# Kernel optimization log

Hardware: AMD Instinct MI355X
Metric: run time of the kernel (lower is better)

Reference implementation:

```python
import jax, jax.numpy as jnp
import numpy as np

N_NODES = 100000
N_EDGES = 1600000
NUM_GRAPHS = 64
D = 128      # num_node_features
H = 256      # hidden_dim
OUT = 1      # output_dim
GA = 6       # num_graph_attributes


def setup_inputs() -> dict:
    key = jax.random.key(0)
    ks = jax.random.split(key, 20)
    p = lambda k, shape: (jax.random.normal(k, shape, jnp.float32) * 0.02)
    return {
        "x": jax.random.normal(ks[0], (N_NODES, D), jnp.float32),
        "edge_index": jax.random.randint(ks[1], (2, N_EDGES), 0, N_NODES),
        "batch": jnp.sort(jax.random.randint(ks[2], (N_NODES,), 0, NUM_GRAPHS)),
        "graph_attr": jax.random.normal(ks[3], (NUM_GRAPHS, GA), jnp.float32),
        # conv1 MLP: Linear(D->H), ReLU, Linear(H->H)
        "w1a": p(ks[4], (D, H)), "b1a": p(ks[5], (H,)),
        "w1b": p(ks[6], (H, H)), "b1b": p(ks[7], (H,)),
        # conv2 MLP: Linear(H->H), ReLU, Linear(H->H)
        "w2a": p(ks[8], (H, H)), "b2a": p(ks[9], (H,)),
        "w2b": p(ks[10], (H, H)), "b2b": p(ks[11], (H,)),
        # head
        "wf1": p(ks[12], (H + GA, H)), "bf1": p(ks[13], (H,)),
        "wf2": p(ks[14], (H, OUT)), "bf2": p(ks[15], (OUT,)),
    }


def _gin_conv(x, src, dst, wa, ba, wb, bb):
    # GINConv with default eps=0: MLP((1+0)*x_i + sum_{j->i} x_j)
    agg = jax.ops.segment_sum(x[src], dst, num_segments=N_NODES)  # [N, d]
    h = x + agg
    h = jax.nn.relu(h @ wa + ba)
    return h @ wb + bb


def reference(x, edge_index, batch, graph_attr,
              w1a, b1a, w1b, b1b, w2a, b2a, w2b, b2b,
              wf1, bf1, wf2, bf2):
    src, dst = edge_index[0], edge_index[1]
    h = jax.nn.relu(_gin_conv(x, src, dst, w1a, b1a, w1b, b1b))  # [N, H]
    h = _gin_conv(h, src, dst, w2a, b2a, w2b, b2b)               # [N, H]
    # global mean pool per graph
    sums = jax.ops.segment_sum(h, batch, num_segments=NUM_GRAPHS)          # [G, H]
    cnts = jax.ops.segment_sum(jnp.ones((h.shape[0], 1), h.dtype), batch,
                               num_segments=NUM_GRAPHS)                    # [G, 1]
    pooled = sums / jnp.maximum(cnts, 1.0)
    g = jnp.concatenate([pooled, graph_attr.reshape(-1, GA)], axis=1)      # [G, H+GA]
    g = jax.nn.relu(g @ wf1 + bf1)
    return g @ wf2 + bf2                                                   # [G, OUT]
```

## Files before the change

kernel.cpp:

```cpp
#include <hip/hip_runtime.h>

#define N_NODES 100000
#define N_EDGES 1600000
#define NGRAPH  64
#define DIN     128
#define HID     256
#define GA      6

#define NBUCK  196
#define BSHIFT 9
#define BCAP   10240

typedef __attribute__((ext_vector_type(8))) short bf16x8;
typedef __attribute__((ext_vector_type(4))) float f32x4;

__device__ __forceinline__ unsigned short f2bf(float f) {
  unsigned int u = __float_as_uint(f);
  u += 0x7fffu + ((u >> 16) & 1u);
  return (unsigned short)(u >> 16);
}
__device__ __forceinline__ float bf_lo(unsigned int u) { return __uint_as_float(u << 16); }
__device__ __forceinline__ float bf_hi(unsigned int u) { return __uint_as_float(u & 0xffff0000u); }
__device__ __forceinline__ unsigned int packbf(float lo, float hi) {
  return (unsigned int)f2bf(lo) | ((unsigned int)f2bf(hi) << 16);
}

__device__ __forceinline__ void gload16(const void* g, void* l) {
  __builtin_amdgcn_global_load_lds(
      (const __attribute__((address_space(1))) unsigned int*)g,
      (__attribute__((address_space(3))) unsigned int*)l, 16, 0, 0);
}


__global__ __launch_bounds__(256) void cvt_all(const float* __restrict__ x,
                                               const float* __restrict__ w1a,
                                               const float* __restrict__ w1b,
                                               const float* __restrict__ w2a,
                                               const float* __restrict__ w2b,
                                               unsigned short* __restrict__ xo,
                                               unsigned short* __restrict__ o1a,
                                               unsigned short* __restrict__ o1b,
                                               unsigned short* __restrict__ o2a,
                                               unsigned short* __restrict__ o2b) {
  int bid = blockIdx.x, tid = threadIdx.x;
  if (bid < 12500) {
    size_t idx = ((size_t)bid * 256 + tid) * 4;
    float4 v = *(const float4*)&x[idx];
    ushort4 o;
    o.x = f2bf(v.x); o.y = f2bf(v.y); o.z = f2bf(v.z); o.w = f2bf(v.w);
    *(ushort4*)&xo[idx] = o;
    return;
  }
  bid -= 12500;
  const float* in; unsigned short* out; int shift, idx;
  if (bid < 128)      { in = w1a; out = o1a; shift = 7; idx = bid * 256 + tid; }
  else if (bid < 384) { in = w1b; out = o1b; shift = 8; idx = (bid - 128) * 256 + tid; }
  else if (bid < 640) { in = w2a; out = o2a; shift = 8; idx = (bid - 384) * 256 + tid; }
  else                { in = w2b; out = o2b; shift = 8; idx = (bid - 640) * 256 + tid; }
  int K = 1 << shift;
  int n = idx >> shift;
  int k = idx & (K - 1);
  out[idx] = f2bf(in[(size_t)k * HID + n]);
}


__global__ __launch_bounds__(256) void bin_kernel(const int* __restrict__ esrc,
                                                  const int* __restrict__ edst,
                                                  int* __restrict__ cursor,
                                                  unsigned int* __restrict__ tmp) {
  __shared__ unsigned int pk[4096];
  __shared__ unsigned char bkb[4096];
  __shared__ int hist[NBUCK], lbase[NBUCK + 1], gbase[NBUCK], lcur[NBUCK];
  const int tid = threadIdx.x;
  const int lane = tid & 63;
  const int ebase = blockIdx.x * 4096;
  const int n = min(4096, N_EDGES - ebase);
  if (tid < NBUCK) hist[tid] = 0;
  __syncthreads();
  unsigned int pkv[16]; int bk[16];
#pragma unroll
  for (int i = 0; i < 16; i++) {
    int e = ebase + i * 256 + tid;
    bk[i] = -1;
    if (e < N_EDGES) {
      int s = esrc[e], d = edst[e];
      bk[i] = d >> BSHIFT;
      pkv[i] = (unsigned int)s | ((unsigned int)(d & ((1 << BSHIFT) - 1)) << 17);
      atomicAdd(&hist[bk[i]], 1);
    }
  }
  __syncthreads();
  if (tid < 64) {
    int i0 = 4 * tid;
    int a0 = (i0 + 0 < NBUCK) ? hist[i0 + 0] : 0;
    int a1 = (i0 + 1 < NBUCK) ? hist[i0 + 1] : 0;
    int a2 = (i0 + 2 < NBUCK) ? hist[i0 + 2] : 0;
    int a3 = (i0 + 3 < NBUCK) ? hist[i0 + 3] : 0;
    int p = a0 + a1 + a2 + a3, sc = p;
#pragma unroll
    for (int off = 1; off < 64; off <<= 1) {
      int t = __shfl_up(sc, off);
      if (lane >= off) sc += t;
    }
    int excl = sc - p;
    if (i0 + 0 < NBUCK) lbase[i0 + 0] = excl;
    if (i0 + 1 < NBUCK) lbase[i0 + 1] = excl + a0;
    if (i0 + 2 < NBUCK) lbase[i0 + 2] = excl + a0 + a1;
    if (i0 + 3 < NBUCK) lbase[i0 + 3] = excl + a0 + a1 + a2;
    if (tid == 63) lbase[NBUCK] = sc;
  }
  __syncthreads();
  if (tid < NBUCK) {
    int c = hist[tid];
    gbase[tid] = c ? atomicAdd(&cursor[tid], c) : 0;
    lcur[tid] = lbase[tid];
  }
  __syncthreads();
#pragma unroll
  for (int i = 0; i < 16; i++) {
    if (bk[i] >= 0) {
      int pos = atomicAdd(&lcur[bk[i]], 1);
      pk[pos] = pkv[i];
      bkb[pos] = (unsigned char)bk[i];
    }
  }
  __syncthreads();
#pragma unroll
  for (int i = 0; i < 16; i++) {
    int idx = i * 256 + tid;
    if (idx < n) {
      int b = bkb[idx];
      tmp[(size_t)b * BCAP + gbase[b] + (idx - lbase[b])] = pk[idx];
    }
  }
}


__global__ __launch_bounds__(512) void sort_kernel(const unsigned int* __restrict__ tmp,
                                                   const int* __restrict__ cnt,
                                                   int* __restrict__ csr,
                                                   int* __restrict__ ssrc) {
  __shared__ int nhist[512], ncur[512];
  __shared__ int bb[NBUCK];
  __shared__ int wsum[8];
  const int b = blockIdx.x;
  const int tid = threadIdx.x;
  const int lane = tid & 63, wid = tid >> 6;
  if (tid < 64) {
    int i0 = 4 * tid;
    int a0 = (i0 + 0 < NBUCK) ? cnt[i0 + 0] : 0;
    int a1 = (i0 + 1 < NBUCK) ? cnt[i0 + 1] : 0;
    int a2 = (i0 + 2 < NBUCK) ? cnt[i0 + 2] : 0;
    int a3 = (i0 + 3 < NBUCK) ? cnt[i0 + 3] : 0;
    int p = a0 + a1 + a2 + a3, sc = p;
#pragma unroll
    for (int off = 1; off < 64; off <<= 1) {
      int t = __shfl_up(sc, off);
      if (lane >= off) sc += t;
    }
    int excl = sc - p;
    if (i0 + 0 < NBUCK) bb[i0 + 0] = excl;
    if (i0 + 1 < NBUCK) bb[i0 + 1] = excl + a0;
    if (i0 + 2 < NBUCK) bb[i0 + 2] = excl + a0 + a1;
    if (i0 + 3 < NBUCK) bb[i0 + 3] = excl + a0 + a1 + a2;
  }
  nhist[tid] = 0;
  __syncthreads();
  const int myCnt = cnt[b];
  const int ebase = bb[b];
  const unsigned int* srcp = tmp + (size_t)b * BCAP;
  for (int i = tid; i < myCnt; i += 512)
    atomicAdd(&nhist[srcp[i] >> 17], 1);
  __syncthreads();
  int v = nhist[tid];
  int sc = v;
#pragma unroll
  for (int off = 1; off < 64; off <<= 1) {
    int t = __shfl_up(sc, off);
    if (lane >= off) sc += t;
  }
  if (lane == 63) wsum[wid] = sc;
  __syncthreads();
  if (tid < 8) {
    int ws = wsum[tid];
#pragma unroll
    for (int off = 1; off < 8; off <<= 1) {
      int t = __shfl_up(ws, off);
      if (tid >= off) ws += t;
    }
    wsum[tid] = ws;
  }
  __syncthreads();
  int excl = ((wid > 0) ? wsum[wid - 1] : 0) + sc - v;
  ncur[tid] = excl;
  int node0 = (b << BSHIFT) + tid;
  if (node0 < N_NODES) csr[node0] = ebase + excl;
  if (b == 0 && tid == 0) csr[N_NODES] = N_EDGES;
  __syncthreads();
  for (int i = tid; i < myCnt; i += 512) {
    unsigned int pe = srcp[i];
    int pos = atomicAdd(&ncur[pe >> 17], 1);
    ssrc[ebase + pos] = (int)(pe & 0x1FFFF);
  }
}


__global__ __launch_bounds__(256) void agg1_kernel(const uint2* __restrict__ x,
                                                   const int* __restrict__ csr,
                                                   const int* __restrict__ ssrc,
                                                   uint2* __restrict__ out) {
  int node = blockIdx.x * 4 + (threadIdx.x >> 6);
  int lane = threadIdx.x & 63;
  int half = lane >> 5;
  int dl   = lane & 31;
  float a0 = 0.f, a1 = 0.f, a2 = 0.f, a3 = 0.f;
  if (half == 0) {
    uint2 u = x[(size_t)node * 32 + dl];
    a0 = bf_lo(u.x); a1 = bf_hi(u.x); a2 = bf_lo(u.y); a3 = bf_hi(u.y);
  }
  int s = csr[node], e = csr[node + 1];
  int i = s;
  for (; i + 8 <= e; i += 8) {
    int s0 = ssrc[i + half],     s1 = ssrc[i + 2 + half];
    int s2 = ssrc[i + 4 + half], s3 = ssrc[i + 6 + half];
    uint2 v0 = x[(size_t)s0 * 32 + dl];
    uint2 v1 = x[(size_t)s1 * 32 + dl];
    uint2 v2 = x[(size_t)s2 * 32 + dl];
    uint2 v3 = x[(size_t)s3 * 32 + dl];
    a0 += bf_lo(v0.x) + bf_lo(v1.x) + bf_lo(v2.x) + bf_lo(v3.x);
    a1 += bf_hi(v0.x) + bf_hi(v1.x) + bf_hi(v2.x) + bf_hi(v3.x);
    a2 += bf_lo(v0.y) + bf_lo(v1.y) + bf_lo(v2.y) + bf_lo(v3.y);
    a3 += bf_hi(v0.y) + bf_hi(v1.y) + bf_hi(v2.y) + bf_hi(v3.y);
  }
  for (; i + 2 <= e; i += 2) {
    int sn = ssrc[i + half];
    uint2 v = x[(size_t)sn * 32 + dl];
    a0 += bf_lo(v.x); a1 += bf_hi(v.x);
    a2 += bf_lo(v.y); a3 += bf_hi(v.y);
  }
  if (i < e && half == 0) {
    uint2 v = x[(size_t)ssrc[i] * 32 + dl];
    a0 += bf_lo(v.x); a1 += bf_hi(v.x);
    a2 += bf_lo(v.y); a3 += bf_hi(v.y);
  }
  a0 += __shfl_xor(a0, 32);
  a1 += __shfl_xor(a1, 32);
  a2 += __shfl_xor(a2, 32);
  a3 += __shfl_xor(a3, 32);
  if (half == 0) {
    uint2 o;
    o.x = packbf(a0, a1);
    o.y = packbf(a2, a3);
    out[(size_t)node * 32 + dl] = o;
  }
}

__global__ __launch_bounds__(256) void agg2_kernel(const uint2* __restrict__ x,
                                                   const int* __restrict__ csr,
                                                   const int* __restrict__ ssrc,
                                                   uint2* __restrict__ out) {
  int node = blockIdx.x * 4 + (threadIdx.x >> 6);
  int lane = threadIdx.x & 63;
  uint2 u = x[(size_t)node * 64 + lane];
  float a0 = bf_lo(u.x), a1 = bf_hi(u.x), a2 = bf_lo(u.y), a3 = bf_hi(u.y);
  int s = csr[node], e = csr[node + 1];
  int i = s;
  for (; i + 8 <= e; i += 8) {
    int n0 = ssrc[i],     n1 = ssrc[i + 1], n2 = ssrc[i + 2], n3 = ssrc[i + 3];
    int n4 = ssrc[i + 4], n5 = ssrc[i + 5], n6 = ssrc[i + 6], n7 = ssrc[i + 7];
    uint2 v0 = x[(size_t)n0 * 64 + lane];
    uint2 v1 = x[(size_t)n1 * 64 + lane];
    uint2 v2 = x[(size_t)n2 * 64 + lane];
    uint2 v3 = x[(size_t)n3 * 64 + lane];
    uint2 v4 = x[(size_t)n4 * 64 + lane];
    uint2 v5 = x[(size_t)n5 * 64 + lane];
    uint2 v6 = x[(size_t)n6 * 64 + lane];
    uint2 v7 = x[(size_t)n7 * 64 + lane];
    a0 += (bf_lo(v0.x) + bf_lo(v1.x)) + (bf_lo(v2.x) + bf_lo(v3.x)) +
          (bf_lo(v4.x) + bf_lo(v5.x)) + (bf_lo(v6.x) + bf_lo(v7.x));
    a1 += (bf_hi(v0.x) + bf_hi(v1.x)) + (bf_hi(v2.x) + bf_hi(v3.x)) +
          (bf_hi(v4.x) + bf_hi(v5.x)) + (bf_hi(v6.x) + bf_hi(v7.x));
    a2 += (bf_lo(v0.y) + bf_lo(v1.y)) + (bf_lo(v2.y) + bf_lo(v3.y)) +
          (bf_lo(v4.y) + bf_lo(v5.y)) + (bf_lo(v6.y) + bf_lo(v7.y));
    a3 += (bf_hi(v0.y) + bf_hi(v1.y)) + (bf_hi(v2.y) + bf_hi(v3.y)) +
          (bf_hi(v4.y) + bf_hi(v5.y)) + (bf_hi(v6.y) + bf_hi(v7.y));
  }
  for (; i < e; i++) {
    uint2 v = x[(size_t)ssrc[i] * 64 + lane];
    a0 += bf_lo(v.x); a1 += bf_hi(v.x);
    a2 += bf_lo(v.y); a3 += bf_hi(v.y);
  }
  uint2 o;
  o.x = packbf(a0, a1);
  o.y = packbf(a2, a3);
  out[(size_t)node * 64 + lane] = o;
}


#define GMAX 4

template<int K, bool RELU, bool POOL>
__global__ __launch_bounds__(512)
void gemm128(const unsigned short* __restrict__ A,
             const unsigned short* __restrict__ Wt,
             const float* __restrict__ bias,
             unsigned short* __restrict__ C,
             const int* __restrict__ batch,
             float* __restrict__ sums) {
  __shared__ unsigned short Asl[128 * 64];
  __shared__ unsigned short Wsl[256 * 64];
  __shared__ float psum[POOL ? GMAX * HID : 1];
  const int tid = threadIdx.x;
  const int lane = tid & 63;
  const int w = tid >> 6;
  const int wm = w >> 2;
  const int wn = w & 3;
  const int l15 = lane & 15, l4 = lane >> 4, l7 = lane & 7;
  const int rowBase = blockIdx.x * 128;

  if (POOL) {
#pragma unroll
    for (int i = tid; i < GMAX * HID; i += 512) psum[i] = 0.f;
  }

  f32x4 acc[4][4] = {};

  for (int k0 = 0; k0 < K; k0 += 64) {
#pragma unroll
    for (int i = 0; i < 2; i++) {
      int c = i * 512 + tid;
      int m = c >> 3, koL = c & 7;
      int koS = koL ^ (m & 7);
      int gr = rowBase + m; if (gr >= N_NODES) gr = N_NODES - 1;
      gload16(&A[(size_t)gr * K + k0 + koS * 8], Asl + (size_t)c * 8);
    }
#pragma unroll
    for (int i = 0; i < 4; i++) {
      int c = i * 512 + tid;
      int n = c >> 3, koL = c & 7;
      int koS = koL ^ (n & 7);
      gload16(&Wt[(size_t)n * K + k0 + koS * 8], Wsl + (size_t)c * 8);
    }
    __syncthreads();
#pragma unroll
    for (int kk = 0; kk < 2; kk++) {
      int koX = (kk * 4 + l4) ^ l7;
      bf16x8 a[4], b[4];
#pragma unroll
      for (int f = 0; f < 4; f++) {
        int rowA = wm * 64 + f * 16 + l15;
        int rowB = wn * 64 + f * 16 + l15;
        a[f] = *(const bf16x8*)&Asl[(size_t)(rowA * 64 + koX * 8)];
        b[f] = *(const bf16x8*)&Wsl[(size_t)(rowB * 64 + koX * 8)];
      }
#pragma unroll
      for (int fm = 0; fm < 4; fm++)
#pragma unroll
        for (int fn = 0; fn < 4; fn++)
          acc[fm][fn] = __builtin_amdgcn_mfma_f32_16x16x32_bf16(a[fm], b[fn], acc[fm][fn], 0, 0, 0);
    }
    __syncthreads();
  }

  if (!POOL) {
#pragma unroll
    for (int fm = 0; fm < 4; fm++) {
      int r0 = rowBase + wm * 64 + fm * 16 + l4 * 4;
#pragma unroll
      for (int fn = 0; fn < 4; fn++) {
        int col = wn * 64 + fn * 16 + l15;
        float bb = bias[col];
#pragma unroll
        for (int j = 0; j < 4; j++) {
          int r = r0 + j;
          if (r < N_NODES) {
            float v = acc[fm][fn][j] + bb;
            if (RELU) v = fmaxf(v, 0.f);
            C[(size_t)r * HID + col] = f2bf(v);
          }
        }
      }
    }
  } else {
    const int g0 = batch[rowBase];
#pragma unroll
    for (int fn = 0; fn < 4; fn++) {
      int col = wn * 64 + fn * 16 + l15;
      float bb = bias[col];
      float part = 0.f;
      int curgi = -1;
#pragma unroll
      for (int fm = 0; fm < 4; fm++) {
#pragma unroll
        for (int j = 0; j < 4; j++) {
          int r = rowBase + wm * 64 + fm * 16 + l4 * 4 + j;
          if (r < N_NODES) {
            float v = acc[fm][fn][j] + bb;
            int gi = batch[r] - g0;
            if (gi != curgi) {
              if (curgi >= 0) {
                if (curgi < GMAX) atomicAdd(&psum[curgi * HID + col], part);
                else atomicAdd(&sums[(size_t)(g0 + curgi) * HID + col], part);
              }
              curgi = gi; part = 0.f;
            }
            part += v;
          }
        }
      }
      if (curgi >= 0) {
        if (curgi < GMAX) atomicAdd(&psum[curgi * HID + col], part);
        else atomicAdd(&sums[(size_t)(g0 + curgi) * HID + col], part);
      }
    }
    __syncthreads();
#pragma unroll
    for (int i = tid; i < GMAX * HID; i += 512) {
      float v = psum[i];
      int g = g0 + (i >> 8);
      if (v != 0.f && g < NGRAPH)
        atomicAdd(&sums[(size_t)g * HID + (i & 255)], v);
    }
  }
}


__global__ __launch_bounds__(256) void head_kernel(const float* __restrict__ sums,
                                                   const int* __restrict__ batch,
                                                   const float* __restrict__ gattr,
                                                   const float* __restrict__ wf1,
                                                   const float* __restrict__ bf1,
                                                   const float* __restrict__ wf2,
                                                   const float* __restrict__ bf2,
                                                   float* __restrict__ out) {
  int g = blockIdx.x, tid = threadIdx.x;
  __shared__ float gv[HID + GA + 2];
  __shared__ float red[256];
  auto lower_bound = [&](int key) {
    int lo = 0, hi = N_NODES;
    while (lo < hi) {
      int mid = (lo + hi) >> 1;
      if (batch[mid] < key) lo = mid + 1; else hi = mid;
    }
    return lo;
  };
  float c = (float)(lower_bound(g + 1) - lower_bound(g));
  c = fmaxf(c, 1.0f);
  gv[tid] = sums[(size_t)g * HID + tid] / c;
  if (tid < GA) gv[HID + tid] = gattr[g * GA + tid];
  if (tid < 2) gv[HID + GA + tid] = 0.f;
  __syncthreads();
  float ac0 = 0.f, ac1 = 0.f, ac2 = 0.f, ac3 = 0.f;
  float ac4 = 0.f, ac5 = 0.f, ac6 = 0.f, ac7 = 0.f;
  const float* wcol = wf1 + tid;
  int k = 0;
#pragma unroll 1
  for (; k + 8 <= HID + GA; k += 8) {
    float w0 = wcol[(size_t)(k + 0) * HID];
    float w1 = wcol[(size_t)(k + 1) * HID];
    float w2 = wcol[(size_t)(k + 2) * HID];
    float w3 = wcol[(size_t)(k + 3) * HID];
    float w4 = wcol[(size_t)(k + 4) * HID];
    float w5 = wcol[(size_t)(k + 5) * HID];
    float w6 = wcol[(size_t)(k + 6) * HID];
    float w7 = wcol[(size_t)(k + 7) * HID];
    ac0 = fmaf(gv[k + 0], w0, ac0);
    ac1 = fmaf(gv[k + 1], w1, ac1);
    ac2 = fmaf(gv[k + 2], w2, ac2);
    ac3 = fmaf(gv[k + 3], w3, ac3);
    ac4 = fmaf(gv[k + 4], w4, ac4);
    ac5 = fmaf(gv[k + 5], w5, ac5);
    ac6 = fmaf(gv[k + 6], w6, ac6);
    ac7 = fmaf(gv[k + 7], w7, ac7);
  }
  for (; k < HID + GA; k++)
    ac0 = fmaf(gv[k], wcol[(size_t)k * HID], ac0);
  float acc = ((ac0 + ac1) + (ac2 + ac3)) + ((ac4 + ac5) + (ac6 + ac7)) + bf1[tid];
  float h = fmaxf(acc, 0.f);
  red[tid] = h * wf2[tid];
  __syncthreads();
  for (int s = 128; s > 0; s >>= 1) {
    if (tid < s) red[tid] += red[tid + s];
    __syncthreads();
  }
  if (tid == 0) out[g] = red[0] + bf2[0];
}


extern "C" void kernel_launch(void* const* d_in, const int* in_sizes, int n_in,
                              void* d_out, int out_size, void* d_ws, size_t ws_size,
                              hipStream_t stream) {
  const float* x     = (const float*)d_in[0];
  const int*   eidx  = (const int*)d_in[1];
  const int*   batch = (const int*)d_in[2];
  const float* gattr = (const float*)d_in[3];
  const float* w1a = (const float*)d_in[4];  const float* b1a = (const float*)d_in[5];
  const float* w1b = (const float*)d_in[6];  const float* b1b = (const float*)d_in[7];
  const float* w2a = (const float*)d_in[8];  const float* b2a = (const float*)d_in[9];
  const float* w2b = (const float*)d_in[10]; const float* b2b = (const float*)d_in[11];
  const float* wf1 = (const float*)d_in[12]; const float* bf1 = (const float*)d_in[13];
  const float* wf2 = (const float*)d_in[14]; const float* bf2 = (const float*)d_in[15];
  float* out = (float*)d_out;

  const int* esrc = eidx;
  const int* edst = eidx + N_EDGES;

  char* w = (char*)d_ws;
  auto alloc = [&](size_t bytes) -> void* {
    void* p = (void*)w;
    w += (bytes + 255) & ~(size_t)255;
    return p;
  };
  unsigned short* B0 = (unsigned short*)alloc((size_t)N_NODES * DIN * 2);
  unsigned short* B1 = (unsigned short*)alloc((size_t)N_NODES * HID * 2);
  unsigned short* B2 = (unsigned short*)alloc((size_t)N_NODES * HID * 2);
  unsigned short* B3 = (unsigned short*)alloc((size_t)N_NODES * HID * 2);
  unsigned short* w1aT = (unsigned short*)alloc(256 * 128 * 2);
  unsigned short* w1bT = (unsigned short*)alloc(256 * 256 * 2);
  unsigned short* w2aT = (unsigned short*)alloc(256 * 256 * 2);
  unsigned short* w2bT = (unsigned short*)alloc(256 * 256 * 2);
  int*   csr    = (int*)alloc((N_NODES + 4) * 4);
  int*   cursor = (int*)alloc(NBUCK * 4);
  unsigned int* tmp = (unsigned int*)alloc((size_t)NBUCK * BCAP * 4);
  int*   ssrc   = (int*)alloc((size_t)N_EDGES * 4);
  float* sums   = (float*)alloc((size_t)NGRAPH * HID * 4);

  hipMemsetAsync(cursor, 0, NBUCK * 4, stream);
  hipMemsetAsync(sums, 0, (size_t)NGRAPH * HID * 4, stream);

  cvt_all<<<12500 + 896, 256, 0, stream>>>(x, w1a, w1b, w2a, w2b,
                                           B0, w1aT, w1bT, w2aT, w2bT);

  bin_kernel<<<(N_EDGES + 4095) / 4096, 256, 0, stream>>>(esrc, edst, cursor, tmp);
  sort_kernel<<<NBUCK, 512, 0, stream>>>(tmp, cursor, csr, ssrc);

  const int ngemm = (N_NODES + 127) / 128;

  agg1_kernel<<<N_NODES / 4, 256, 0, stream>>>((const uint2*)B0, csr, ssrc, (uint2*)B1);
  gemm128<128, true, false><<<ngemm, 512, 0, stream>>>(B1, w1aT, b1a, B3, nullptr, nullptr);
  gemm128<256, true, false><<<ngemm, 512, 0, stream>>>(B3, w1bT, b1b, B2, nullptr, nullptr);
  agg2_kernel<<<N_NODES / 4, 256, 0, stream>>>((const uint2*)B2, csr, ssrc, (uint2*)B1);
  gemm128<256, true, false><<<ngemm, 512, 0, stream>>>(B1, w2aT, b2a, B3, nullptr, nullptr);
  gemm128<256, false, true><<<ngemm, 512, 0, stream>>>(B3, w2bT, b2b, nullptr, batch, sums);

  head_kernel<<<NGRAPH, 256, 0, stream>>>(sums, batch, gattr, wf1, bf1, wf2, bf2, out);
}
```

Measured before the change: 403.6 us.

## Fuse edge binning into conversion kernel and halve bucket size for sort

Edge binning now shares one launch with the bf16 conversion of x and the weights: the first NBIN blocks do binning and the remaining blocks do conversion. The two memsets become one contiguous memset by placing sums right after cursor. Buckets shrink from 512 to 256 destination nodes, doubling their count to 391, so the sort kernel runs more blocks, each with a smaller per-node histogram. This cuts launch overhead and fills more compute units in the sort stage. In exchange, more blocks hit the global cursor atomics, and half the threads in each sort block sit idle during the prefix scan.

```diff
diff --git a/kernel.cpp b/kernel.cpp
--- a/kernel.cpp
+++ b/kernel.cpp
@@ -7,9 +7,11 @@
 #define HID     256
 #define GA      6
 
-#define NBUCK  196
-#define BSHIFT 9
-#define BCAP   10240
+#define NBUCK  391
+#define BSHIFT 8
+#define BCAP   6144
+#define NCVT   13396
+#define NBIN   391
 
 typedef __attribute__((ext_vector_type(8))) short bf16x8;
 typedef __attribute__((ext_vector_type(4))) float f32x4;
@@ -32,7 +34,11 @@
 }
 
 
-__global__ __launch_bounds__(256) void cvt_all(const float* __restrict__ x,
+__global__ __launch_bounds__(256) void cvt_bin(const int* __restrict__ esrc,
+                                               const int* __restrict__ edst,
+                                               int* __restrict__ cursor,
+                                               unsigned int* __restrict__ tmp,
+                                               const float* __restrict__ x,
                                                const float* __restrict__ w1a,
                                                const float* __restrict__ w1b,
                                                const float* __restrict__ w2a,
@@ -42,40 +48,38 @@
                                                unsigned short* __restrict__ o1b,
                                                unsigned short* __restrict__ o2a,
                                                unsigned short* __restrict__ o2b) {
+  __shared__ unsigned int pk[4096];
+  __shared__ unsigned short bkb[4096];
+  __shared__ int hist[NBUCK], lbase[NBUCK + 1], gbase[NBUCK], lcur[NBUCK];
   int bid = blockIdx.x, tid = threadIdx.x;
-  if (bid < 12500) {
-    size_t idx = ((size_t)bid * 256 + tid) * 4;
-    float4 v = *(const float4*)&x[idx];
-    ushort4 o;
-    o.x = f2bf(v.x); o.y = f2bf(v.y); o.z = f2bf(v.z); o.w = f2bf(v.w);
-    *(ushort4*)&xo[idx] = o;
+
+  if (bid >= NBIN) {
+    bid -= NBIN;
+    if (bid < 12500) {
+      size_t idx = ((size_t)bid * 256 + tid) * 4;
+      float4 v = *(const float4*)&x[idx];
+      ushort4 o;
+      o.x = f2bf(v.x); o.y = f2bf(v.y); o.z = f2bf(v.z); o.w = f2bf(v.w);
+      *(ushort4*)&xo[idx] = o;
+      return;
+    }
+    bid -= 12500;
+    const float* in; unsigned short* out; int shift, idx;
+    if (bid < 128)      { in = w1a; out = o1a; shift = 7; idx = bid * 256 + tid; }
+    else if (bid < 384) { in = w1b; out = o1b; shift = 8; idx = (bid - 128) * 256 + tid; }
+    else if (bid < 640) { in = w2a; out = o2a; shift = 8; idx = (bid - 384) * 256 + tid; }
+    else                { in = w2b; out = o2b; shift = 8; idx = (bid - 640) * 256 + tid; }
+    int K = 1 << shift;
+    int n = idx >> shift;
+    int k = idx & (K - 1);
+    out[idx] = f2bf(in[(size_t)k * HID + n]);
     return;
   }
-  bid -= 12500;
-  const float* in; unsigned short* out; int shift, idx;
-  if (bid < 128)      { in = w1a; out = o1a; shift = 7; idx = bid * 256 + tid; }
-  else if (bid < 384) { in = w1b; out = o1b; shift = 8; idx = (bid - 128) * 256 + tid; }
-  else if (bid < 640) { in = w2a; out = o2a; shift = 8; idx = (bid - 384) * 256 + tid; }
-  else                { in = w2b; out = o2b; shift = 8; idx = (bid - 640) * 256 + tid; }
-  int K = 1 << shift;
-  int n = idx >> shift;
-  int k = idx & (K - 1);
-  out[idx] = f2bf(in[(size_t)k * HID + n]);
-}
-
-
-__global__ __launch_bounds__(256) void bin_kernel(const int* __restrict__ esrc,
-                                                  const int* __restrict__ edst,
-                                                  int* __restrict__ cursor,
-                                                  unsigned int* __restrict__ tmp) {
-  __shared__ unsigned int pk[4096];
-  __shared__ unsigned char bkb[4096];
-  __shared__ int hist[NBUCK], lbase[NBUCK + 1], gbase[NBUCK], lcur[NBUCK];
-  const int tid = threadIdx.x;
+
   const int lane = tid & 63;
-  const int ebase = blockIdx.x * 4096;
+  const int ebase = bid * 4096;
   const int n = min(4096, N_EDGES - ebase);
-  if (tid < NBUCK) hist[tid] = 0;
+  for (int i = tid; i < NBUCK; i += 256) hist[i] = 0;
   __syncthreads();
   unsigned int pkv[16]; int bk[16];
 #pragma unroll
@@ -91,29 +95,32 @@
   }
   __syncthreads();
   if (tid < 64) {
-    int i0 = 4 * tid;
-    int a0 = (i0 + 0 < NBUCK) ? hist[i0 + 0] : 0;
-    int a1 = (i0 + 1 < NBUCK) ? hist[i0 + 1] : 0;
-    int a2 = (i0 + 2 < NBUCK) ? hist[i0 + 2] : 0;
-    int a3 = (i0 + 3 < NBUCK) ? hist[i0 + 3] : 0;
-    int p = a0 + a1 + a2 + a3, sc = p;
+    int i0 = 8 * tid;
+    int a[8], s = 0;
+#pragma unroll
+    for (int k = 0; k < 8; k++) {
+      a[k] = (i0 + k < NBUCK) ? hist[i0 + k] : 0;
+      s += a[k];
+    }
+    int sc = s;
 #pragma unroll
     for (int off = 1; off < 64; off <<= 1) {
       int t = __shfl_up(sc, off);
       if (lane >= off) sc += t;
     }
-    int excl = sc - p;
-    if (i0 + 0 < NBUCK) lbase[i0 + 0] = excl;
-    if (i0 + 1 < NBUCK) lbase[i0 + 1] = excl + a0;
-    if (i0 + 2 < NBUCK) lbase[i0 + 2] = excl + a0 + a1;
-    if (i0 + 3 < NBUCK) lbase[i0 + 3] = excl + a0 + a1 + a2;
+    int excl = sc - s;
+#pragma unroll
+    for (int k = 0; k < 8; k++) {
+      if (i0 + k < NBUCK) lbase[i0 + k] = excl;
+      excl += a[k];
+    }
     if (tid == 63) lbase[NBUCK] = sc;
   }
   __syncthreads();
-  if (tid < NBUCK) {
-    int c = hist[tid];
-    gbase[tid] = c ? atomicAdd(&cursor[tid], c) : 0;
-    lcur[tid] = lbase[tid];
+  for (int i = tid; i < NBUCK; i += 256) {
+    int c = hist[i];
+    gbase[i] = c ? atomicAdd(&cursor[i], c) : 0;
+    lcur[i] = lbase[i];
   }
   __syncthreads();
 #pragma unroll
@@ -121,7 +128,7 @@
     if (bk[i] >= 0) {
       int pos = atomicAdd(&lcur[bk[i]], 1);
       pk[pos] = pkv[i];
-      bkb[pos] = (unsigned char)bk[i];
+      bkb[pos] = (unsigned short)bk[i];
     }
   }
   __syncthreads();
@@ -140,31 +147,34 @@
                                                    const int* __restrict__ cnt,
                                                    int* __restrict__ csr,
                                                    int* __restrict__ ssrc) {
-  __shared__ int nhist[512], ncur[512];
+  __shared__ int nhist[256], ncur[256];
   __shared__ int bb[NBUCK];
-  __shared__ int wsum[8];
+  __shared__ int wsum[4];
   const int b = blockIdx.x;
   const int tid = threadIdx.x;
   const int lane = tid & 63, wid = tid >> 6;
   if (tid < 64) {
-    int i0 = 4 * tid;
-    int a0 = (i0 + 0 < NBUCK) ? cnt[i0 + 0] : 0;
-    int a1 = (i0 + 1 < NBUCK) ? cnt[i0 + 1] : 0;
-    int a2 = (i0 + 2 < NBUCK) ? cnt[i0 + 2] : 0;
-    int a3 = (i0 + 3 < NBUCK) ? cnt[i0 + 3] : 0;
-    int p = a0 + a1 + a2 + a3, sc = p;
+    int i0 = 8 * tid;
+    int a[8], s = 0;
+#pragma unroll
+    for (int k = 0; k < 8; k++) {
+      a[k] = (i0 + k < NBUCK) ? cnt[i0 + k] : 0;
+      s += a[k];
+    }
+    int sc = s;
 #pragma unroll
     for (int off = 1; off < 64; off <<= 1) {
       int t = __shfl_up(sc, off);
       if (lane >= off) sc += t;
     }
-    int excl = sc - p;
-    if (i0 + 0 < NBUCK) bb[i0 + 0] = excl;
-    if (i0 + 1 < NBUCK) bb[i0 + 1] = excl + a0;
-    if (i0 + 2 < NBUCK) bb[i0 + 2] = excl + a0 + a1;
-    if (i0 + 3 < NBUCK) bb[i0 + 3] = excl + a0 + a1 + a2;
-  }
-  nhist[tid] = 0;
+    int excl = sc - s;
+#pragma unroll
+    for (int k = 0; k < 8; k++) {
+      if (i0 + k < NBUCK) bb[i0 + k] = excl;
+      excl += a[k];
+    }
+  }
+  if (tid < 256) nhist[tid] = 0;
   __syncthreads();
   const int myCnt = cnt[b];
   const int ebase = bb[b];
@@ -172,29 +182,34 @@
   for (int i = tid; i < myCnt; i += 512)
     atomicAdd(&nhist[srcp[i] >> 17], 1);
   __syncthreads();
-  int v = nhist[tid];
-  int sc = v;
-#pragma unroll
-  for (int off = 1; off < 64; off <<= 1) {
-    int t = __shfl_up(sc, off);
-    if (lane >= off) sc += t;
-  }
-  if (lane == 63) wsum[wid] = sc;
-  __syncthreads();
-  if (tid < 8) {
+  int v = 0, sc = 0;
+  if (tid < 256) {
+    v = nhist[tid];
+    sc = v;
+#pragma unroll
+    for (int off = 1; off < 64; off <<= 1) {
+      int t = __shfl_up(sc, off);
+      if (lane >= off) sc += t;
+    }
+    if (lane == 63) wsum[wid] = sc;
+  }
+  __syncthreads();
+  if (tid < 4) {
     int ws = wsum[tid];
 #pragma unroll
-    for (int off = 1; off < 8; off <<= 1) {
+    for (int off = 1; off < 4; off <<= 1) {
       int t = __shfl_up(ws, off);
       if (tid >= off) ws += t;
     }
     wsum[tid] = ws;
   }
   __syncthreads();
-  int excl = ((wid > 0) ? wsum[wid - 1] : 0) + sc - v;
-  ncur[tid] = excl;
-  int node0 = (b << BSHIFT) + tid;
-  if (node0 < N_NODES) csr[node0] = ebase + excl;
+  if (tid < 256) {
+    int excl = ((wid > 0) ? wsum[wid - 1] : 0) + sc - v;
+    ncur[tid] = excl;
+    int node0 = (b << BSHIFT) + tid;
+    if (node0 < N_NODES) csr[node0] = ebase + excl;
+  }
   if (b == 0 && tid == 0) csr[N_NODES] = N_EDGES;
   __syncthreads();
   for (int i = tid; i < myCnt; i += 512) {
@@ -521,17 +536,16 @@
   unsigned short* w2bT = (unsigned short*)alloc(256 * 256 * 2);
   int*   csr    = (int*)alloc((N_NODES + 4) * 4);
   int*   cursor = (int*)alloc(NBUCK * 4);
+  float* sums   = (float*)alloc((size_t)NGRAPH * HID * 4);
   unsigned int* tmp = (unsigned int*)alloc((size_t)NBUCK * BCAP * 4);
   int*   ssrc   = (int*)alloc((size_t)N_EDGES * 4);
-  float* sums   = (float*)alloc((size_t)NGRAPH * HID * 4);
-
-  hipMemsetAsync(cursor, 0, NBUCK * 4, stream);
-  hipMemsetAsync(sums, 0, (size_t)NGRAPH * HID * 4, stream);
-
-  cvt_all<<<12500 + 896, 256, 0, stream>>>(x, w1a, w1b, w2a, w2b,
+
+  size_t zbytes = ((NBUCK * 4 + 255) & ~(size_t)255) + (size_t)NGRAPH * HID * 4;
+  hipMemsetAsync(cursor, 0, zbytes, stream);
+
+  cvt_bin<<<NBIN + NCVT, 256, 0, stream>>>(esrc, edst, cursor, tmp,
+                                           x, w1a, w1b, w2a, w2b,
                                            B0, w1aT, w1bT, w2aT, w2bT);
-
-  bin_kernel<<<(N_EDGES + 4095) / 4096, 256, 0, stream>>>(esrc, edst, cursor, tmp);
   sort_kernel<<<NBUCK, 512, 0, stream>>>(tmp, cursor, csr, ssrc);
 
   const int ngemm = (N_NODES + 127) / 128;
```

Result: faster. 388.5 us (-3.7%).
